# Optimization experiments

Hardware: AMD Instinct MI355X
Metric: run time of the kernel (lower is better)

## Reference

```python
import jax, jax.numpy as jnp
import numpy as np

V = 100000   # num_vertices
E = 3200000  # directed edges (symmetric: both directions of E//2 undirected edges)
B = 8        # batch of meshes
C = 3        # xyz vertex features


def setup_inputs() -> dict:
    key = jax.random.key(0)
    k1, k2, k3, k4 = jax.random.split(key, 4)
    src = jax.random.randint(k1, (E // 2,), 0, V, dtype=jnp.int32)
    dst = jax.random.randint(k2, (E // 2,), 0, V, dtype=jnp.int32)
    edge_index = jnp.stack([jnp.concatenate([src, dst]),
                            jnp.concatenate([dst, src])])  # (2, E)
    features = jax.random.normal(k3, (B, V, C), dtype=jnp.float32)
    target_features = jax.random.normal(k4, (B, V, C), dtype=jnp.float32)
    return {"features": features, "target_features": target_features,
            "edge_index": edge_index}


def _sym_laplacian(edge_index, num_nodes, dtype):
    """get_laplacian(..., normalization='sym'): L = I - D^{-1/2} A D^{-1/2}.
    Returns (lap_row, lap_col, lap_weight) as edge list with self-loops appended."""
    row, col = edge_index
    ones = jnp.ones(row.shape, dtype)
    deg = jax.ops.segment_sum(ones, row, num_segments=num_nodes)
    deg_inv_sqrt = jnp.where(deg > 0, deg, 1.0) ** -0.5
    deg_inv_sqrt = jnp.where(deg > 0, deg_inv_sqrt, 0.0)
    ew = -deg_inv_sqrt[row] * deg_inv_sqrt[col]
    loop = jnp.arange(num_nodes, dtype=row.dtype)
    lap_row = jnp.concatenate([row, loop])
    lap_col = jnp.concatenate([col, loop])
    lap_w = jnp.concatenate([ew, jnp.ones((num_nodes,), dtype)])
    return lap_row, lap_col, lap_w


def _apply_laplacian(x, lap_row, lap_col, lap_w, num_nodes):
    # x: (B, V, C) -> gather on source vertex, scale, scatter_add on target vertex
    xt = jnp.swapaxes(x, 0, 1)                       # (V, B, C)
    msg = xt[lap_row] * lap_w[:, None, None]          # (E+V, B, C)
    out = jax.ops.segment_sum(msg, lap_col, num_segments=num_nodes)  # (V, B, C)
    return jnp.swapaxes(out, 0, 1)                    # (B, V, C)


def reference(features, target_features, edge_index):
    lap_row, lap_col, lap_w = _sym_laplacian(edge_index, V, features.dtype)
    lap_x = _apply_laplacian(features, lap_row, lap_col, lap_w, V)
    lap_y = _apply_laplacian(target_features, lap_row, lap_col, lap_w, V)
    # per-batch mse averaged over batch == global mean since shapes are uniform
    return jnp.mean((lap_x - lap_y) ** 2)
```

## Files before the change

### kernel.cpp

```cpp
#include <hip/hip_runtime.h>

#define C_CONST 3
#define B_CONST 8
#define BC 24
#define ROWB 32
#define VP 196
#define NP 512
#define CAP 6784
#define K1_T 512
#define K1_PPT 8
#define K1_PPB (K1_T * K1_PPT)
#define K1_EPB (K1_PPB * 2)
#define GT 1024
#define KREG 7
#define GSPLIT 8

typedef float floatx2 __attribute__((ext_vector_type(2)));

__global__ __launch_bounds__(K1_T) void bucket_kernel(
    const int* __restrict__ row, const int* __restrict__ col, int E2,
    int* __restrict__ pcount, unsigned int* __restrict__ bucket)
{
    __shared__ unsigned int sl[K1_EPB];
    __shared__ int hist[NP];
    __shared__ int offs[NP];
    __shared__ int gbase[NP];
    __shared__ int wsum[8];
    int tid = threadIdx.x;
    hist[tid] = 0;
    __syncthreads();

    int p0 = blockIdx.x * K1_PPB + tid * K1_PPT;
    unsigned int pk[2 * K1_PPT];
    unsigned int pack[2 * K1_PPT];
    if (p0 + K1_PPT <= E2) {
#pragma unroll
        for (int q = 0; q < K1_PPT / 4; q++) {
            int4 rv = *(const int4*)(row + p0 + q * 4);
            int4 cv = *(const int4*)(col + p0 + q * 4);
            int rr[4] = {rv.x, rv.y, rv.z, rv.w};
            int cc[4] = {cv.x, cv.y, cv.z, cv.w};
#pragma unroll
            for (int j = 0; j < 4; j++) {
                int i = (q * 4 + j) * 2;
                int r = rr[j], c = cc[j];
                int pc = c / VP;
                pk[i] = (unsigned int)r | ((unsigned int)(c - pc * VP) << 17);
                int rk0 = atomicAdd(&hist[pc], 1);
                pack[i] = (unsigned int)pc | ((unsigned int)rk0 << 9);
                int pr = r / VP;
                pk[i + 1] = (unsigned int)c | ((unsigned int)(r - pr * VP) << 17);
                int rk1 = atomicAdd(&hist[pr], 1);
                pack[i + 1] = (unsigned int)pr | ((unsigned int)rk1 << 9);
            }
        }
    } else {
#pragma unroll
        for (int j = 0; j < K1_PPT; j++) {
            int i = j * 2;
            int e = p0 + j;
            if (e < E2) {
                int r = row[e], c = col[e];
                int pc = c / VP;
                pk[i] = (unsigned int)r | ((unsigned int)(c - pc * VP) << 17);
                int rk0 = atomicAdd(&hist[pc], 1);
                pack[i] = (unsigned int)pc | ((unsigned int)rk0 << 9);
                int pr = r / VP;
                pk[i + 1] = (unsigned int)c | ((unsigned int)(r - pr * VP) << 17);
                int rk1 = atomicAdd(&hist[pr], 1);
                pack[i + 1] = (unsigned int)pr | ((unsigned int)rk1 << 9);
            } else { pk[i] = 0; pack[i] = 0xFFFFFFFFu;
                     pk[i + 1] = 0; pack[i + 1] = 0xFFFFFFFFu; }
        }
    }
    __syncthreads();

    int lane = tid & 63, wid = tid >> 6;
    int hv = hist[tid];
    int sv = hv;
#pragma unroll
    for (int off = 1; off < 64; off <<= 1) {
        int t = __shfl_up(sv, off, 64);
        if (lane >= off) sv += t;
    }
    if (lane == 63) wsum[wid] = sv;
    __syncthreads();
    if (tid < 64) {
        int w = (tid < 8) ? wsum[tid] : 0;
#pragma unroll
        for (int off = 1; off < 8; off <<= 1) {
            int t = __shfl_up(w, off, 64);
            if (tid >= off) w += t;
        }
        if (tid < 8) wsum[tid] = w;
    }
    __syncthreads();
    offs[tid] = (wid ? wsum[wid - 1] : 0) + sv - hv;
    gbase[tid] = (hv > 0) ? atomicAdd(&pcount[tid], hv) : 0;
    __syncthreads();

#pragma unroll
    for (int i = 0; i < 2 * K1_PPT; i++) {
        unsigned int pc = pack[i];
        if (pc != 0xFFFFFFFFu)
            sl[offs[pc & 511u] + (pc >> 9)] = pk[i];
    }
    __syncthreads();

    int sub = lane >> 4, li = lane & 15;
    for (int pp0 = wid * (NP / 8); pp0 < (wid + 1) * (NP / 8); pp0 += 4) {
        int pp = pp0 + sub;
        int cnt = hist[pp], lo = offs[pp], gb = gbase[pp];
        unsigned int* dst = bucket + (size_t)pp * CAP;
        for (int i = li; i < cnt; i += 16) {
            int pos = gb + i;
            if (pos < CAP) dst[pos] = sl[lo + i];
        }
    }
}

#define PREP_T 1024
__global__ __launch_bounds__(PREP_T) void prep_kernel(
    const int* __restrict__ pcount, const unsigned int* __restrict__ bucket,
    const float* __restrict__ x, const float* __restrict__ y, int V,
    unsigned char* __restrict__ wh)
{
    __shared__ int cnt[VP];
    __shared__ float ssc[VP];
    __shared__ unsigned char tile[VP * ROWB];
    int p = blockIdx.x;
    int tid = threadIdx.x;
    for (int i = tid; i < VP; i += PREP_T) cnt[i] = 0;
    __syncthreads();
    int n = pcount[p]; if (n > CAP) n = CAP;
    const unsigned int* bp = bucket + (size_t)p * CAP;
    for (int i = tid; i < n; i += PREP_T) atomicAdd(&cnt[bp[i] >> 17], 1);
    __syncthreads();
    int vb = p * VP;
    int nv = V - vb; if (nv > VP) nv = VP; if (nv < 0) nv = 0;
    for (int i = tid; i < nv; i += PREP_T) {
        int dg = cnt[i];
        ssc[i] = (dg > 0) ? rsqrtf((float)dg) : 1.0f;
    }
    __syncthreads();

    int ns = nv * C_CONST;
    int ns4 = ns >> 2;
    for (int idx = tid; idx < B_CONST * ns4; idx += PREP_T) {
        int b = idx / ns4;
        int q = idx - b * ns4;
        size_t off = ((size_t)b * V + vb) * C_CONST + (size_t)q * 4;
        float4 xv = *(const float4*)(x + off);
        float4 yv = *(const float4*)(y + off);
        float vals[4] = {xv.x - yv.x, xv.y - yv.y, xv.z - yv.z, xv.w - yv.w};
        int f0 = q * 4;
#pragma unroll
        for (int j = 0; j < 4; j++) {
            int f = f0 + j;
            int vl = f / C_CONST;
            int c = f - vl * C_CONST;
            float w = ssc[vl] * vals[j];
            int packed = __builtin_amdgcn_cvt_pk_fp8_f32(w, w, 0, false);
            tile[vl * ROWB + b * C_CONST + c] = (unsigned char)(packed & 0xFF);
        }
    }
    __syncthreads();

    int nbytes = nv * ROWB;
    uint4* dst = (uint4*)(wh + (size_t)vb * ROWB);
    const uint4* srcT = (const uint4*)tile;
    for (int i = tid; i < (nbytes >> 4); i += PREP_T) dst[i] = srcT[i];
}

__global__ __launch_bounds__(GT) void gather_loss_kernel(
    const int* __restrict__ pcount, const unsigned int* __restrict__ bucket,
    const unsigned char* __restrict__ wh, int V, float inv_n, float* __restrict__ out)
{
    __shared__ unsigned int sorted[CAP];
    __shared__ int rowptr[VP + 1];
    __shared__ int cur[VP];
    __shared__ int wsum[4];
    __shared__ float ls[16];
    int p = blockIdx.x;
    int tid = threadIdx.x;
    int n = pcount[p]; if (n > CAP) n = CAP;
    const unsigned int* bp = bucket + (size_t)p * CAP;

    unsigned int ent[KREG];
    int rk[KREG];
#pragma unroll
    for (int k = 0; k < KREG; k++) {
        int i = tid + k * GT;
        ent[k] = (i < n) ? bp[i] : 0xFFFFFFFFu;
    }

    for (int i = tid; i < VP; i += GT) cur[i] = 0;
    __syncthreads();
#pragma unroll
    for (int k = 0; k < KREG; k++)
        rk[k] = (ent[k] != 0xFFFFFFFFu) ? atomicAdd(&cur[ent[k] >> 17], 1) : 0;
    __syncthreads();

    int lane = tid & 63, wid = tid >> 6;
    int cv = 0, sv = 0;
    if (tid < 256) {
        cv = (tid < VP) ? cur[tid] : 0;
        sv = cv;
#pragma unroll
        for (int off = 1; off < 64; off <<= 1) {
            int t = __shfl_up(sv, off, 64);
            if (lane >= off) sv += t;
        }
        if (lane == 63) wsum[wid] = sv;
    }
    __syncthreads();
    if (tid < 64) {
        int w = (tid < 4) ? wsum[tid] : 0;
#pragma unroll
        for (int off = 1; off < 4; off <<= 1) {
            int t = __shfl_up(w, off, 64);
            if (tid >= off) w += t;
        }
        if (tid < 4) wsum[tid] = w;
    }
    __syncthreads();
    if (tid < VP) {
        rowptr[tid + 1] = sv + (wid ? wsum[wid - 1] : 0);
        if (tid == 0) rowptr[0] = 0;
    }
    __syncthreads();

#pragma unroll
    for (int k = 0; k < KREG; k++) {
        unsigned int e = ent[k];
        if (e != 0xFFFFFFFFu) {
            int cl = e >> 17;
            sorted[rowptr[cl] + rk[k]] = e & 0x1FFFFu;
        }
    }
    __syncthreads();

    float s = 0.0f;
    for (int item = tid; item < VP * GSPLIT; item += GT) {
        int cl = item >> 3, g = item & 7;
        int v = p * VP + cl;
        if (v < V) {
            int q0 = rowptr[cl], q1 = rowptr[cl + 1];
            float acc[24];
#pragma unroll
            for (int i = 0; i < 24; i++) acc[i] = 0.0f;
            int q = q0 + g;
            int r_cur = (q < q1) ? (int)sorted[q] : 0;
            for (; q < q1; q += GSPLIT) {
                int qn = q + GSPLIT;
                int r_nxt = (qn < q1) ? (int)sorted[qn] : 0;
                const unsigned char* rb = wh + ((size_t)r_cur << 5);
                uint4 w0 = *(const uint4*)rb;
                uint2 w1 = *(const uint2*)(rb + 16);
                unsigned int wd[6] = {w0.x, w0.y, w0.z, w0.w, w1.x, w1.y};
#pragma unroll
                for (int t = 0; t < 6; t++) {
                    floatx2 lo = __builtin_amdgcn_cvt_pk_f32_fp8((int)wd[t], false);
                    floatx2 hi = __builtin_amdgcn_cvt_pk_f32_fp8((int)wd[t], true);
                    acc[t*4+0] += lo.x; acc[t*4+1] += lo.y;
                    acc[t*4+2] += hi.x; acc[t*4+3] += hi.y;
                }
                r_cur = r_nxt;
            }
#pragma unroll
            for (int i = 0; i < 24; i++) {
                acc[i] += __shfl_xor(acc[i], 1, 64);
                acc[i] += __shfl_xor(acc[i], 2, 64);
                acc[i] += __shfl_xor(acc[i], 4, 64);
            }
            if (g == 0) {
                int dg = q1 - q0;
                float dvv = (dg > 0) ? rsqrtf((float)dg) : 0.0f;
                float di  = (dg > 0) ? sqrtf((float)dg)  : 1.0f;
                const unsigned char* sb = wh + ((size_t)v << 5);
                uint4 s0 = *(const uint4*)sb;
                uint2 s1 = *(const uint2*)(sb + 16);
                unsigned int sd[6] = {s0.x, s0.y, s0.z, s0.w, s1.x, s1.y};
#pragma unroll
                for (int t = 0; t < 6; t++) {
                    floatx2 lo = __builtin_amdgcn_cvt_pk_f32_fp8((int)sd[t], false);
                    floatx2 hi = __builtin_amdgcn_cvt_pk_f32_fp8((int)sd[t], true);
                    float r0 = lo.x * di - dvv * acc[t*4+0];
                    float r1 = lo.y * di - dvv * acc[t*4+1];
                    float r2 = hi.x * di - dvv * acc[t*4+2];
                    float r3 = hi.y * di - dvv * acc[t*4+3];
                    s += r0*r0 + r1*r1 + r2*r2 + r3*r3;
                }
            }
        }
    }

    for (int off = 32; off > 0; off >>= 1) s += __shfl_down(s, off, 64);
    if (lane == 0) ls[wid] = s;
    __syncthreads();
    if (tid == 0) {
        float tot = 0.0f;
        for (int i = 0; i < GT / 64; i++) tot += ls[i];
        atomicAdd(out, tot * inv_n);
    }
}

extern "C" void kernel_launch(void* const* d_in, const int* in_sizes, int n_in,
                              void* d_out, int out_size, void* d_ws, size_t ws_size,
                              hipStream_t stream) {
    const float* x = (const float*)d_in[0];
    const float* y = (const float*)d_in[1];
    const int*  ei = (const int*)d_in[2];

    const int E = in_sizes[2] / 2;
    const int E2 = E / 2;
    const int V = in_sizes[0] / (B_CONST * C_CONST);
    const int* row = ei;
    const int* col = ei + E;

    char* ws = (char*)d_ws;
    size_t off = 0;
    unsigned int* bucket = (unsigned int*)(ws + off); off += (size_t)NP * CAP * 4;
    unsigned char* wh = (unsigned char*)(ws + off);   off += (size_t)NP * VP * ROWB;
    int* pcount = (int*)(ws + off);                   off += (size_t)NP * 4;
    float* outf = (float*)d_out;

    hipMemsetAsync(pcount, 0, (size_t)NP * sizeof(int), stream);
    hipMemsetAsync(d_out, 0, sizeof(float), stream);

    bucket_kernel<<<(E2 + K1_PPB - 1) / K1_PPB, K1_T, 0, stream>>>(row, col, E2, pcount, bucket);
    prep_kernel<<<NP, PREP_T, 0, stream>>>(pcount, bucket, x, y, V, wh);
    gather_loss_kernel<<<NP, GT, 0, stream>>>(pcount, bucket, wh, V,
                                              1.0f / (float)(V * BC), outf);
}
```

Baseline: 135.6 us.

## Move per-partition counting sort into prep kernel and replace memsets with zero kernel

The per-partition counting sort (histogram, scan, scatter) moves out of the gather/loss kernel into the prep kernel, which already histogrammed the bucket for degrees. The sorted column list and row pointers go to global workspace for the gather kernel to load. This removes duplicate bucket reading and atomics from the gather kernel and shrinks its shared-memory footprint. In exchange, the sorted array makes an extra global write and read round trip. The two memset calls become a single tiny zero kernel to cut launch overhead.

After: 136.8 us. Within noise of the previous version (+0.9%).

```diff
diff --git a/kernel.cpp b/kernel.cpp
--- a/kernel.cpp
+++ b/kernel.cpp
@@ -11,11 +11,19 @@
 #define K1_PPT 8
 #define K1_PPB (K1_T * K1_PPT)
 #define K1_EPB (K1_PPB * 2)
+#define PREP_T 1024
 #define GT 1024
 #define KREG 7
 #define GSPLIT 8
 
 typedef float floatx2 __attribute__((ext_vector_type(2)));
+
+__global__ __launch_bounds__(NP) void zero_kernel(int* __restrict__ pcount,
+                                                  float* __restrict__ out)
+{
+    pcount[threadIdx.x] = 0;
+    if (threadIdx.x == 0) *out = 0.0f;
+}
 
 __global__ __launch_bounds__(K1_T) void bucket_kernel(
     const int* __restrict__ row, const int* __restrict__ col, int E2,
@@ -119,33 +127,83 @@
     }
 }
 
-#define PREP_T 1024
-__global__ __launch_bounds__(PREP_T) void prep_kernel(
+__global__ __launch_bounds__(PREP_T) void prep_sort_kernel(
     const int* __restrict__ pcount, const unsigned int* __restrict__ bucket,
     const float* __restrict__ x, const float* __restrict__ y, int V,
-    unsigned char* __restrict__ wh)
+    unsigned char* __restrict__ wh, unsigned int* __restrict__ gsorted,
+    int* __restrict__ growptr)
 {
-    __shared__ int cnt[VP];
+    __shared__ unsigned int sorted[CAP];
+    __shared__ int rowptr[VP + 1];
+    __shared__ int cur[VP];
+    __shared__ int wsum[4];
     __shared__ float ssc[VP];
     __shared__ unsigned char tile[VP * ROWB];
     int p = blockIdx.x;
     int tid = threadIdx.x;
-    for (int i = tid; i < VP; i += PREP_T) cnt[i] = 0;
-    __syncthreads();
     int n = pcount[p]; if (n > CAP) n = CAP;
     const unsigned int* bp = bucket + (size_t)p * CAP;
-    for (int i = tid; i < n; i += PREP_T) atomicAdd(&cnt[bp[i] >> 17], 1);
-    __syncthreads();
+
+    unsigned int ent[KREG];
+    int rk[KREG];
+#pragma unroll
+    for (int k = 0; k < KREG; k++) {
+        int i = tid + k * PREP_T;
+        ent[k] = (i < n) ? bp[i] : 0xFFFFFFFFu;
+    }
+    for (int i = tid; i < VP; i += PREP_T) cur[i] = 0;
+    __syncthreads();
+#pragma unroll
+    for (int k = 0; k < KREG; k++)
+        rk[k] = (ent[k] != 0xFFFFFFFFu) ? atomicAdd(&cur[ent[k] >> 17], 1) : 0;
+    __syncthreads();
+
+    int lane = tid & 63, wid = tid >> 6;
+    int sv = 0;
+    if (tid < 256) {
+        int cv = (tid < VP) ? cur[tid] : 0;
+        sv = cv;
+#pragma unroll
+        for (int off = 1; off < 64; off <<= 1) {
+            int t = __shfl_up(sv, off, 64);
+            if (lane >= off) sv += t;
+        }
+        if (lane == 63) wsum[wid] = sv;
+    }
+    __syncthreads();
+    if (tid < 64) {
+        int w = (tid < 4) ? wsum[tid] : 0;
+#pragma unroll
+        for (int off = 1; off < 4; off <<= 1) {
+            int t = __shfl_up(w, off, 64);
+            if (tid >= off) w += t;
+        }
+        if (tid < 4) wsum[tid] = w;
+    }
+    __syncthreads();
+    if (tid < VP) {
+        rowptr[tid + 1] = sv + (wid ? wsum[wid - 1] : 0);
+        if (tid == 0) rowptr[0] = 0;
+    }
+    __syncthreads();
+
+#pragma unroll
+    for (int k = 0; k < KREG; k++) {
+        unsigned int e = ent[k];
+        if (e != 0xFFFFFFFFu) {
+            int cl = e >> 17;
+            sorted[rowptr[cl] + rk[k]] = e & 0x1FFFFu;
+        }
+    }
+    if (tid < VP) {
+        int dg = rowptr[tid + 1] - rowptr[tid];
+        ssc[tid] = (dg > 0) ? rsqrtf((float)dg) : 1.0f;
+    }
+    __syncthreads();
+
     int vb = p * VP;
     int nv = V - vb; if (nv > VP) nv = VP; if (nv < 0) nv = 0;
-    for (int i = tid; i < nv; i += PREP_T) {
-        int dg = cnt[i];
-        ssc[i] = (dg > 0) ? rsqrtf((float)dg) : 1.0f;
-    }
-    __syncthreads();
-
-    int ns = nv * C_CONST;
-    int ns4 = ns >> 2;
+    int ns4 = (nv * C_CONST) >> 2;
     for (int idx = tid; idx < B_CONST * ns4; idx += PREP_T) {
         int b = idx / ns4;
         int q = idx - b * ns4;
@@ -170,74 +228,26 @@
     uint4* dst = (uint4*)(wh + (size_t)vb * ROWB);
     const uint4* srcT = (const uint4*)tile;
     for (int i = tid; i < (nbytes >> 4); i += PREP_T) dst[i] = srcT[i];
+    unsigned int* gs = gsorted + (size_t)p * CAP;
+    for (int i = tid; i < n; i += PREP_T) gs[i] = sorted[i];
+    if (tid < VP + 1) growptr[p * (VP + 1) + tid] = rowptr[tid];
 }
 
 __global__ __launch_bounds__(GT) void gather_loss_kernel(
-    const int* __restrict__ pcount, const unsigned int* __restrict__ bucket,
+    const unsigned int* __restrict__ gsorted, const int* __restrict__ growptr,
     const unsigned char* __restrict__ wh, int V, float inv_n, float* __restrict__ out)
 {
     __shared__ unsigned int sorted[CAP];
     __shared__ int rowptr[VP + 1];
-    __shared__ int cur[VP];
-    __shared__ int wsum[4];
     __shared__ float ls[16];
     int p = blockIdx.x;
     int tid = threadIdx.x;
-    int n = pcount[p]; if (n > CAP) n = CAP;
-    const unsigned int* bp = bucket + (size_t)p * CAP;
-
-    unsigned int ent[KREG];
-    int rk[KREG];
-#pragma unroll
-    for (int k = 0; k < KREG; k++) {
-        int i = tid + k * GT;
-        ent[k] = (i < n) ? bp[i] : 0xFFFFFFFFu;
-    }
-
-    for (int i = tid; i < VP; i += GT) cur[i] = 0;
-    __syncthreads();
-#pragma unroll
-    for (int k = 0; k < KREG; k++)
-        rk[k] = (ent[k] != 0xFFFFFFFFu) ? atomicAdd(&cur[ent[k] >> 17], 1) : 0;
-    __syncthreads();
-
-    int lane = tid & 63, wid = tid >> 6;
-    int cv = 0, sv = 0;
-    if (tid < 256) {
-        cv = (tid < VP) ? cur[tid] : 0;
-        sv = cv;
-#pragma unroll
-        for (int off = 1; off < 64; off <<= 1) {
-            int t = __shfl_up(sv, off, 64);
-            if (lane >= off) sv += t;
-        }
-        if (lane == 63) wsum[wid] = sv;
-    }
-    __syncthreads();
-    if (tid < 64) {
-        int w = (tid < 4) ? wsum[tid] : 0;
-#pragma unroll
-        for (int off = 1; off < 4; off <<= 1) {
-            int t = __shfl_up(w, off, 64);
-            if (tid >= off) w += t;
-        }
-        if (tid < 4) wsum[tid] = w;
-    }
-    __syncthreads();
-    if (tid < VP) {
-        rowptr[tid + 1] = sv + (wid ? wsum[wid - 1] : 0);
-        if (tid == 0) rowptr[0] = 0;
-    }
-    __syncthreads();
-
-#pragma unroll
-    for (int k = 0; k < KREG; k++) {
-        unsigned int e = ent[k];
-        if (e != 0xFFFFFFFFu) {
-            int cl = e >> 17;
-            sorted[rowptr[cl] + rk[k]] = e & 0x1FFFFu;
-        }
-    }
+
+    if (tid < VP + 1) rowptr[tid] = growptr[p * (VP + 1) + tid];
+    __syncthreads();
+    int n = rowptr[VP];
+    const unsigned int* gs = gsorted + (size_t)p * CAP;
+    for (int i = tid; i < n; i += GT) sorted[i] = gs[i];
     __syncthreads();
 
     float s = 0.0f;
@@ -296,6 +306,7 @@
     }
 
     for (int off = 32; off > 0; off >>= 1) s += __shfl_down(s, off, 64);
+    int lane = tid & 63, wid = tid >> 6;
     if (lane == 0) ls[wid] = s;
     __syncthreads();
     if (tid == 0) {
@@ -320,16 +331,16 @@
 
     char* ws = (char*)d_ws;
     size_t off = 0;
-    unsigned int* bucket = (unsigned int*)(ws + off); off += (size_t)NP * CAP * 4;
-    unsigned char* wh = (unsigned char*)(ws + off);   off += (size_t)NP * VP * ROWB;
-    int* pcount = (int*)(ws + off);                   off += (size_t)NP * 4;
+    unsigned int* bucket = (unsigned int*)(ws + off);  off += (size_t)NP * CAP * 4;
+    unsigned int* gsorted = (unsigned int*)(ws + off); off += (size_t)NP * CAP * 4;
+    unsigned char* wh = (unsigned char*)(ws + off);    off += (size_t)NP * VP * ROWB;
+    int* growptr = (int*)(ws + off);                   off += (size_t)NP * (VP + 1) * 4;
+    int* pcount = (int*)(ws + off);                    off += (size_t)NP * 4;
     float* outf = (float*)d_out;
 
-    hipMemsetAsync(pcount, 0, (size_t)NP * sizeof(int), stream);
-    hipMemsetAsync(d_out, 0, sizeof(float), stream);
-
+    zero_kernel<<<1, NP, 0, stream>>>(pcount, outf);
     bucket_kernel<<<(E2 + K1_PPB - 1) / K1_PPB, K1_T, 0, stream>>>(row, col, E2, pcount, bucket);
-    prep_kernel<<<NP, PREP_T, 0, stream>>>(pcount, bucket, x, y, V, wh);
-    gather_loss_kernel<<<NP, GT, 0, stream>>>(pcount, bucket, wh, V,
+    prep_sort_kernel<<<NP, PREP_T, 0, stream>>>(pcount, bucket, x, y, V, wh, gsorted, growptr);
+    gather_loss_kernel<<<NP, GT, 0, stream>>>(gsorted, growptr, wh, V,
                                               1.0f / (float)(V * BC), outf);
 }
```
